# Kernel tuning notes

Hardware: AMD Instinct MI355X
Metric: run time of the kernel (lower is better)

Reference implementation:

```python
import jax, jax.numpy as jnp
import numpy as np

N = 100000  # number of nodes
SELF_LOOP_W = 2.0  # improved=True in PyG GCNConv


def gcn_conv(x, edge_index, W, b):
    # x: [N, Fin], edge_index: [2, E] (row=src, col=dst), W: [Fin, Fout], b: [Fout]
    src, dst = edge_index[0], edge_index[1]
    h = x @ W  # [N, Fout]
    # degree with improved self-loops (weight 2.0)
    ones = jnp.ones(src.shape, dtype=h.dtype)
    deg = jax.ops.segment_sum(ones, dst, num_segments=N) + SELF_LOOP_W
    dinv = jnp.where(deg > 0, jax.lax.rsqrt(deg), 0.0)
    norm = dinv[src] * dinv[dst]  # [E]
    agg = jax.ops.segment_sum(h[src] * norm[:, None], dst, num_segments=N)
    # self-loop contribution: weight 2.0, norm = dinv_i * 2 * dinv_i
    agg = agg + h * (SELF_LOOP_W * dinv * dinv)[:, None]
    return agg + b


def setup_inputs() -> dict:
    key = jax.random.key(0)
    ks = jax.random.split(key, 6)
    x = jax.random.normal(ks[0], (N, 64), dtype=jnp.float32)
    edge_index = jax.random.randint(ks[1], (2, 1600000), 0, N, dtype=jnp.int64)
    W1 = jax.random.normal(ks[2], (64, 64), dtype=jnp.float32) * 0.1
    b1 = jax.random.normal(ks[3], (64,), dtype=jnp.float32) * 0.1
    W2 = jax.random.normal(ks[4], (64, 32), dtype=jnp.float32) * 0.1
    b2 = jax.random.normal(ks[5], (32,), dtype=jnp.float32) * 0.1
    return {"x": x, "edge_index": edge_index, "W1": W1, "b1": b1, "W2": W2, "b2": b2}


def reference(x, edge_index, W1, b1, W2, b2):
    h1 = jax.nn.relu(gcn_conv(x, edge_index, W1, b1))
    feature_map = h1
    out = gcn_conv(h1, edge_index, W2, b2)
    return (out, feature_map)
```

## Files before the change

kernel.cpp:

```cpp
#include <hip/hip_runtime.h>

#define N_NODES 100000
#define E_EDGES 1600000

#define BSHIFT 7
#define BSIZE 128
#define NBUCK ((N_NODES + BSIZE - 1) / BSIZE)
#define STAGE_TPB 512
#define STAGE_EPT 8
#define STAGE_CHUNK (STAGE_TPB * STAGE_EPT)
#define NREP 2
#define BUCKET_CAP 4096
#define CSR_STRIDE (BUCKET_CAP + 512)

typedef __attribute__((ext_vector_type(8))) short short8;
typedef __attribute__((ext_vector_type(4))) float float4v;
typedef __attribute__((ext_vector_type(4))) int int4v;
typedef __attribute__((ext_vector_type(4))) unsigned uint4v;

__device__ inline unsigned short f2bf(float f) {
    union { float f; unsigned u; } t; t.f = f;
    unsigned r = (t.u + 0x7fffu + ((t.u >> 16) & 1u)) >> 16;
    return (unsigned short)r;
}
__device__ inline float bf2f(unsigned short h) {
    union { unsigned u; float f; } t; t.u = ((unsigned)h) << 16; return t.f;
}
__device__ inline unsigned pack_bf16x2(float a, float b) {
    return (unsigned)f2bf(a) | ((unsigned)f2bf(b) << 16);
}
__device__ inline float bf_lo(unsigned u) { union { unsigned u; float f; } t; t.u = u << 16; return t.f; }
__device__ inline float bf_hi(unsigned u) { union { unsigned u; float f; } t; t.u = u & 0xffff0000u; return t.f; }

__global__ void cursor_init_kernel(int* __restrict__ gcursor,
                                   unsigned* __restrict__ HS1, unsigned* __restrict__ HS2) {
    int b = blockIdx.x * blockDim.x + threadIdx.x;
    if (b < NBUCK) gcursor[b] = b * BUCKET_CAP;
    if (b < 32) HS1[(size_t)N_NODES * 32 + b] = 0u;
    if (b < 16) HS2[(size_t)N_NODES * 16 + b] = 0u;
}

__global__ void __launch_bounds__(STAGE_TPB) stage_kernel(
    const int* __restrict__ src, const int* __restrict__ dst,
    int* __restrict__ gcursor, unsigned* __restrict__ staged, int E) {
    __shared__ int hist[NREP][NBUCK];
    __shared__ int dbase[NBUCK];
    __shared__ int scanw[1024];
    __shared__ unsigned lrec[STAGE_CHUNK];
    __shared__ int laddr[STAGE_CHUNK];
    const int tid = threadIdx.x;
    const int rep = (tid >> 8) & (NREP - 1);
    const int e0 = blockIdx.x * STAGE_CHUNK;
    for (int i = tid; i < NREP * NBUCK; i += STAGE_TPB) ((int*)hist)[i] = 0;
    scanw[tid] = 0; scanw[tid + 512] = 0;
    __syncthreads();
    int d[STAGE_EPT], s[STAGE_EPT];
#pragma unroll
    for (int k = 0; k < STAGE_EPT / 4; ++k) {
        int e = e0 + (k * STAGE_TPB + tid) * 4;
        if (e < E) {
            int4v sv = __builtin_nontemporal_load((const int4v*)(src + e));
            int4v dv = __builtin_nontemporal_load((const int4v*)(dst + e));
#pragma unroll
            for (int i = 0; i < 4; ++i) {
                s[4 * k + i] = sv[i];
                d[4 * k + i] = dv[i];
                atomicAdd(&hist[rep][dv[i] >> BSHIFT], 1);
            }
        } else {
#pragma unroll
            for (int i = 0; i < 4; ++i) d[4 * k + i] = -1;
        }
    }
    __syncthreads();
    for (int i = tid; i < NBUCK; i += STAGE_TPB) scanw[i] = hist[0][i] + hist[1][i];
    if (tid + 512 < NBUCK) scanw[tid + 512] = hist[0][tid + 512] + hist[1][tid + 512];
    __syncthreads();
    for (int off = 1; off < 1024; off <<= 1) {
        int v0 = (tid >= off) ? scanw[tid - off] : 0;
        int v1 = (tid + 512 >= off) ? scanw[tid + 512 - off] : 0;
        __syncthreads();
        scanw[tid] += v0;
        scanw[tid + 512] += v1;
        __syncthreads();
    }
    for (int i = tid; i < NBUCK; i += STAGE_TPB) {
        int h0 = hist[0][i], h1 = hist[1][i];
        int t = h0 + h1;
        int excl = scanw[i] - t;
        if (t > 0) {
            int g = atomicAdd(&gcursor[i], t);
            dbase[i] = g - excl;
        }
        hist[0][i] = excl;
        hist[1][i] = excl + h0;
    }
    __syncthreads();
#pragma unroll
    for (int k = 0; k < STAGE_EPT; ++k) {
        if (d[k] >= 0) {
            int b = d[k] >> BSHIFT;
            int slot = atomicAdd(&hist[rep][b], 1);
            lrec[slot] = (unsigned)s[k] | ((unsigned)(d[k] & (BSIZE - 1)) << 17);
            laddr[slot] = dbase[b] + slot;
        }
    }
    __syncthreads();
    const int total = min(STAGE_CHUNK, E - e0);
    for (int i = tid; i < total; i += STAGE_TPB) {
        int a = laddr[i];
        if ((unsigned)a < (unsigned)(NBUCK * BUCKET_CAP))
            staged[a] = lrec[i];
    }
}

__global__ void bucket_csr_kernel(const unsigned* __restrict__ staged,
                                  const int* __restrict__ gcursor,
                                  int4v* __restrict__ meta, float* __restrict__ dinv,
                                  int* __restrict__ csrc, int n) {
    __shared__ int ldeg[BSIZE];
    __shared__ int laex[BSIZE];
    __shared__ int lscan[BSIZE];
    __shared__ int lcnt[BSIZE];
    __shared__ int h2[32];
    __shared__ int c2[32];
    __shared__ unsigned lrec[BUCKET_CAP];
    __shared__ int lsrc[BUCKET_CAP + 512];
    __shared__ int ltot;
    const int b = blockIdx.x;
    const int node0 = b * BSIZE;
    const int nn = min(BSIZE, n - node0);
    const int tid = threadIdx.x;
    if (tid < BSIZE) { ldeg[tid] = 0; lcnt[tid] = 0; }
    if (tid < 32) { h2[tid] = 0; c2[tid] = 0; }
    __syncthreads();
    const int ebase = b * CSR_STRIDE;
    int ecnt = gcursor[b] - b * BUCKET_CAP;
    if (ecnt > BUCKET_CAP) ecnt = BUCKET_CAP;
    const int sbase = b * BUCKET_CAP;
    for (int i = tid; i < ecnt; i += 256) {
        unsigned r = staged[sbase + i];
        lrec[i] = r;
        atomicAdd(&ldeg[(r >> 17) & (BSIZE - 1)], 1);
    }
    __syncthreads();
    int mydeg = (tid < BSIZE) ? ldeg[tid] : 0;
    int adeg = (mydeg + 3) & ~3;
    if (tid < BSIZE) lscan[tid] = adeg;
    __syncthreads();
    for (int off = 1; off < BSIZE; off <<= 1) {
        int v = 0;
        if (tid < BSIZE && tid >= off) v = lscan[tid - off];
        __syncthreads();
        if (tid < BSIZE) lscan[tid] += v;
        __syncthreads();
    }
    const int bin = min(adeg >> 2, 31);
    float mydinv = 0.0f;
    if (tid < BSIZE) {
        int aex = lscan[tid] - adeg;
        laex[tid] = aex;
        if (tid == BSIZE - 1) ltot = lscan[tid];
        if (tid < nn) {
            mydinv = rsqrtf((float)mydeg + 2.0f);
            dinv[node0 + tid] = mydinv;
            for (int k = mydeg; k < adeg; ++k) lsrc[aex + k] = N_NODES;
            atomicAdd(&h2[bin], 1);
        }
    }
    __syncthreads();
    if (tid == 0) {
        int acc = 0;
        for (int k = 0; k < 32; ++k) { int v = h2[k]; h2[k] = acc; acc += v; }
    }
    __syncthreads();
    if (tid < nn) {
        int pos = h2[bin] + atomicAdd(&c2[bin], 1);
        union { float f; int i; } dv; dv.f = mydinv;
        meta[node0 + pos] = (int4v){ebase + laex[tid], mydeg, node0 + tid, dv.i};
    }
    for (int i = tid; i < ecnt; i += 256) {
        unsigned r = lrec[i];
        int dl = (int)((r >> 17) & (BSIZE - 1));
        int sv = (int)(r & 0x1FFFFu);
        int pos = laex[dl] + atomicAdd(&lcnt[dl], 1);
        if (pos < BUCKET_CAP + 512) lsrc[pos] = sv;
    }
    __syncthreads();
    const int tot = ltot;
    for (int i = tid; i < tot; i += 256)
        csrc[ebase + i] = lsrc[i];
}

template <int FOUT>
__global__ void __launch_bounds__(256) linear_mfma_kernel(
    const float* __restrict__ X, const float* __restrict__ W,
    const float* __restrict__ dinv, unsigned* __restrict__ HS, int n) {
    constexpr int NT = FOUT / 16;
    constexpr int ROWU = NT * 8;
    const int NTILES_M = n / 16;
    const int lane = threadIdx.x & 63;
    const int gwave = blockIdx.x * 4 + (threadIdx.x >> 6);
    const int nwaves = gridDim.x * 4;
    const int m = lane & 15;
    const int q = lane >> 4;

    short8 Bhi[2][NT], Blo[2][NT];
#pragma unroll
    for (int ks = 0; ks < 2; ++ks)
#pragma unroll
        for (int nt = 0; nt < NT; ++nt) {
            short8 bh, bl;
#pragma unroll
            for (int j = 0; j < 8; ++j) {
                int k = ks * 32 + q * 8 + j;
                float wv = W[k * FOUT + nt * 16 + m];
                unsigned short h = f2bf(wv);
                bh[j] = (short)h;
                bl[j] = (short)f2bf(wv - bf2f(h));
            }
            Bhi[ks][nt] = bh;
            Blo[ks][nt] = bl;
        }

    for (int tile = gwave; tile < NTILES_M; tile += nwaves) {
        const int row0 = tile * 16;
        float4v C[NT];
#pragma unroll
        for (int nt = 0; nt < NT; ++nt) C[nt] = (float4v){0.f, 0.f, 0.f, 0.f};
#pragma unroll
        for (int ks = 0; ks < 2; ++ks) {
            const float* xp = X + (size_t)(row0 + m) * 64 + ks * 32 + q * 8;
            float4v x0 = __builtin_nontemporal_load((const float4v*)xp);
            float4v x1 = __builtin_nontemporal_load((const float4v*)(xp + 4));
            short8 Ahi, Alo;
#pragma unroll
            for (int j = 0; j < 4; ++j) {
                unsigned short h0 = f2bf(x0[j]);
                Ahi[j] = (short)h0;
                Alo[j] = (short)f2bf(x0[j] - bf2f(h0));
                unsigned short h1 = f2bf(x1[j]);
                Ahi[4 + j] = (short)h1;
                Alo[4 + j] = (short)f2bf(x1[j] - bf2f(h1));
            }
#pragma unroll
            for (int nt = 0; nt < NT; ++nt) {
                C[nt] = __builtin_amdgcn_mfma_f32_16x16x32_bf16(Ahi, Bhi[ks][nt], C[nt], 0, 0, 0);
                C[nt] = __builtin_amdgcn_mfma_f32_16x16x32_bf16(Alo, Bhi[ks][nt], C[nt], 0, 0, 0);
                C[nt] = __builtin_amdgcn_mfma_f32_16x16x32_bf16(Ahi, Blo[ks][nt], C[nt], 0, 0, 0);
            }
        }
#pragma unroll
        for (int ch = 0; ch < NT / 2; ++ch) {
#pragma unroll
            for (int reg = 0; reg < 4; ++reg) {
                int r = row0 + q * 4 + reg;
                float di = dinv[r];
                unsigned u = pack_bf16x2(C[2 * ch][reg] * di, C[2 * ch + 1][reg] * di);
                __builtin_nontemporal_store(u, HS + (size_t)r * ROWU + ch * 16 + m);
            }
        }
    }
}

template <int ROWU, bool RELU>
__global__ void __launch_bounds__(256) gather_vec_kernel(
    const int4v* __restrict__ meta, const int* __restrict__ csrc,
    const unsigned* __restrict__ HS, const float* __restrict__ bias,
    float* __restrict__ OUT, int n) {
    constexpr int G = ROWU / 4;
    constexpr int NPB = 256 / G;
    constexpr int FOUT = ROWU * 2;
    const int gslot = blockIdx.x * NPB + (int)(threadIdx.x / G);
    const int t = threadIdx.x % G;
    if (gslot >= n) return;
    const int4v mi = meta[gslot];
    const int start = mi[0];
    const int deg = mi[1];
    const int node = mi[2];
    union { int i; float f; } dv; dv.i = mi[3];
    const float dd = dv.f;
    const int pend = start + ((deg + 3) & ~3);
    const unsigned* __restrict__ HSt = HS + 4 * t;
    const uint4v own = *(const uint4v*)(HS + (size_t)node * ROWU + 4 * t);
    float alo[4], ahi[4];
#pragma unroll
    for (int k = 0; k < 4; ++k) { alo[k] = 2.0f * bf_lo(own[k]); ahi[k] = 2.0f * bf_hi(own[k]); }
    int j = start;
    for (; j + 8 <= pend; j += 8) {
        int4v s0 = __builtin_nontemporal_load((const int4v*)(csrc + j));
        int4v s1 = __builtin_nontemporal_load((const int4v*)(csrc + j + 4));
        uint4v u0 = *(const uint4v*)(HSt + (size_t)s0[0] * ROWU);
        uint4v u1 = *(const uint4v*)(HSt + (size_t)s0[1] * ROWU);
        uint4v u2 = *(const uint4v*)(HSt + (size_t)s0[2] * ROWU);
        uint4v u3 = *(const uint4v*)(HSt + (size_t)s0[3] * ROWU);
        uint4v u4 = *(const uint4v*)(HSt + (size_t)s1[0] * ROWU);
        uint4v u5 = *(const uint4v*)(HSt + (size_t)s1[1] * ROWU);
        uint4v u6 = *(const uint4v*)(HSt + (size_t)s1[2] * ROWU);
        uint4v u7 = *(const uint4v*)(HSt + (size_t)s1[3] * ROWU);
#pragma unroll
        for (int k = 0; k < 4; ++k) {
            float l01 = bf_lo(u0[k]) + bf_lo(u1[k]);
            float l23 = bf_lo(u2[k]) + bf_lo(u3[k]);
            float l45 = bf_lo(u4[k]) + bf_lo(u5[k]);
            float l67 = bf_lo(u6[k]) + bf_lo(u7[k]);
            alo[k] += (l01 + l23) + (l45 + l67);
            float h01 = bf_hi(u0[k]) + bf_hi(u1[k]);
            float h23 = bf_hi(u2[k]) + bf_hi(u3[k]);
            float h45 = bf_hi(u4[k]) + bf_hi(u5[k]);
            float h67 = bf_hi(u6[k]) + bf_hi(u7[k]);
            ahi[k] += (h01 + h23) + (h45 + h67);
        }
    }
    if (j < pend) {
        int4v s0 = __builtin_nontemporal_load((const int4v*)(csrc + j));
        uint4v u0 = *(const uint4v*)(HSt + (size_t)s0[0] * ROWU);
        uint4v u1 = *(const uint4v*)(HSt + (size_t)s0[1] * ROWU);
        uint4v u2 = *(const uint4v*)(HSt + (size_t)s0[2] * ROWU);
        uint4v u3 = *(const uint4v*)(HSt + (size_t)s0[3] * ROWU);
#pragma unroll
        for (int k = 0; k < 4; ++k) {
            alo[k] += (bf_lo(u0[k]) + bf_lo(u1[k])) + (bf_lo(u2[k]) + bf_lo(u3[k]));
            ahi[k] += (bf_hi(u0[k]) + bf_hi(u1[k])) + (bf_hi(u2[k]) + bf_hi(u3[k]));
        }
    }
    const int ch = t >> 2;
    const int c0 = (4 * t) & 15;
    const float4v blv = *(const float4v*)(bias + 32 * ch + c0);
    const float4v bhv = *(const float4v*)(bias + 32 * ch + 16 + c0);
    float4v olo, ohi;
#pragma unroll
    for (int k = 0; k < 4; ++k) {
        float o0 = alo[k] * dd + blv[k];
        float o1 = ahi[k] * dd + bhv[k];
        if (RELU) { o0 = fmaxf(o0, 0.0f); o1 = fmaxf(o1, 0.0f); }
        olo[k] = o0;
        ohi[k] = o1;
    }
    float* op = OUT + (size_t)node * FOUT + 32 * ch + c0;
    __builtin_nontemporal_store(olo, (float4v*)op);
    __builtin_nontemporal_store(ohi, (float4v*)(op + 16));
}

extern "C" void kernel_launch(void* const* d_in, const int* in_sizes, int n_in,
                              void* d_out, int out_size, void* d_ws, size_t ws_size,
                              hipStream_t stream) {
    const float* x  = (const float*)d_in[0];
    const int*   ei = (const int*)d_in[1];
    const float* W1 = (const float*)d_in[2];
    const float* b1 = (const float*)d_in[3];
    const float* W2 = (const float*)d_in[4];
    const float* b2 = (const float*)d_in[5];

    const int* srcp = ei;
    const int* dstp = ei + E_EDGES;

    float* out = (float*)d_out;
    float* fm  = (float*)d_out + N_NODES * 32;

    char* w = (char*)d_ws;
    auto alloc = [&w](size_t bytes) -> void* {
        uintptr_t p = ((uintptr_t)w + 255) & ~(uintptr_t)255;
        w = (char*)(p + bytes);
        return (void*)p;
    };
    int*      gcursor  = (int*)alloc(sizeof(int) * NBUCK);
    int4v*    meta     = (int4v*)alloc(sizeof(int4v) * N_NODES);
    float*    dinv     = (float*)alloc(sizeof(float) * N_NODES);
    int*      csrc     = (int*)alloc(sizeof(int) * (size_t)NBUCK * CSR_STRIDE);
    unsigned* staged   = (unsigned*)alloc(sizeof(unsigned) * (size_t)NBUCK * BUCKET_CAP);
    unsigned* HS1      = (unsigned*)alloc(sizeof(unsigned) * (size_t)(N_NODES + 1) * 32);
    unsigned* HS2      = (unsigned*)alloc(sizeof(unsigned) * (size_t)(N_NODES + 1) * 16);

    cursor_init_kernel<<<(NBUCK + 255) / 256, 256, 0, stream>>>(gcursor, HS1, HS2);
    stage_kernel<<<(E_EDGES + STAGE_CHUNK - 1) / STAGE_CHUNK, STAGE_TPB, 0, stream>>>(
        srcp, dstp, gcursor, staged, E_EDGES);
    bucket_csr_kernel<<<NBUCK, 256, 0, stream>>>(staged, gcursor, meta, dinv, csrc, N_NODES);

    linear_mfma_kernel<64><<<512, 256, 0, stream>>>(x, W1, dinv, HS1, N_NODES);
    gather_vec_kernel<32, true><<<(N_NODES + 31) / 32, 256, 0, stream>>>(
        meta, csrc, HS1, b1, fm, N_NODES);

    linear_mfma_kernel<32><<<512, 256, 0, stream>>>(fm, W2, dinv, HS2, N_NODES);
    gather_vec_kernel<16, false><<<(N_NODES + 63) / 64, 256, 0, stream>>>(
        meta, csrc, HS2, b2, out, N_NODES);
}
```

Baseline: 199.2 us.

## Reuse first-pass atomic ranks for scatter slots and drop cursor init kernel

The return value of the histogram atomicAdd is now kept as a per-edge rank in both the staging and bucket-CSR kernels. Scatter positions are then computed from the prefix offsets plus that rank, which removes the second round of shared-memory atomics. The cursor init kernel is replaced by a hipMemsetAsync, with bucket bases folded into dbase, and the sentinel row zeroing moves into the linear kernel. Nontemporal load and store hints are added for the staged and CSR buffers. The cost is an extra per-edge rank array in registers and LDS.

```diff
diff --git a/kernel.cpp b/kernel.cpp
--- a/kernel.cpp
+++ b/kernel.cpp
@@ -32,18 +32,11 @@
 __device__ inline float bf_lo(unsigned u) { union { unsigned u; float f; } t; t.u = u << 16; return t.f; }
 __device__ inline float bf_hi(unsigned u) { union { unsigned u; float f; } t; t.u = u & 0xffff0000u; return t.f; }
 
-__global__ void cursor_init_kernel(int* __restrict__ gcursor,
-                                   unsigned* __restrict__ HS1, unsigned* __restrict__ HS2) {
-    int b = blockIdx.x * blockDim.x + threadIdx.x;
-    if (b < NBUCK) gcursor[b] = b * BUCKET_CAP;
-    if (b < 32) HS1[(size_t)N_NODES * 32 + b] = 0u;
-    if (b < 16) HS2[(size_t)N_NODES * 16 + b] = 0u;
-}
-
 __global__ void __launch_bounds__(STAGE_TPB) stage_kernel(
     const int* __restrict__ src, const int* __restrict__ dst,
     int* __restrict__ gcursor, unsigned* __restrict__ staged, int E) {
     __shared__ int hist[NREP][NBUCK];
+    __shared__ int excl[NBUCK];
     __shared__ int dbase[NBUCK];
     __shared__ int scanw[1024];
     __shared__ unsigned lrec[STAGE_CHUNK];
@@ -52,9 +45,8 @@
     const int rep = (tid >> 8) & (NREP - 1);
     const int e0 = blockIdx.x * STAGE_CHUNK;
     for (int i = tid; i < NREP * NBUCK; i += STAGE_TPB) ((int*)hist)[i] = 0;
-    scanw[tid] = 0; scanw[tid + 512] = 0;
-    __syncthreads();
-    int d[STAGE_EPT], s[STAGE_EPT];
+    __syncthreads();
+    int d[STAGE_EPT], s[STAGE_EPT], rk[STAGE_EPT];
 #pragma unroll
     for (int k = 0; k < STAGE_EPT / 4; ++k) {
         int e = e0 + (k * STAGE_TPB + tid) * 4;
@@ -65,7 +57,7 @@
             for (int i = 0; i < 4; ++i) {
                 s[4 * k + i] = sv[i];
                 d[4 * k + i] = dv[i];
-                atomicAdd(&hist[rep][dv[i] >> BSHIFT], 1);
+                rk[4 * k + i] = atomicAdd(&hist[rep][dv[i] >> BSHIFT], 1);
             }
         } else {
 #pragma unroll
@@ -73,8 +65,8 @@
         }
     }
     __syncthreads();
-    for (int i = tid; i < NBUCK; i += STAGE_TPB) scanw[i] = hist[0][i] + hist[1][i];
-    if (tid + 512 < NBUCK) scanw[tid + 512] = hist[0][tid + 512] + hist[1][tid + 512];
+    scanw[tid] = (tid < NBUCK) ? hist[0][tid] + hist[1][tid] : 0;
+    scanw[tid + 512] = (tid + 512 < NBUCK) ? hist[0][tid + 512] + hist[1][tid + 512] : 0;
     __syncthreads();
     for (int off = 1; off < 1024; off <<= 1) {
         int v0 = (tid >= off) ? scanw[tid - off] : 0;
@@ -85,22 +77,20 @@
         __syncthreads();
     }
     for (int i = tid; i < NBUCK; i += STAGE_TPB) {
-        int h0 = hist[0][i], h1 = hist[1][i];
-        int t = h0 + h1;
-        int excl = scanw[i] - t;
+        int t = hist[0][i] + hist[1][i];
+        int ex = scanw[i] - t;
+        excl[i] = ex;
         if (t > 0) {
             int g = atomicAdd(&gcursor[i], t);
-            dbase[i] = g - excl;
-        }
-        hist[0][i] = excl;
-        hist[1][i] = excl + h0;
+            dbase[i] = i * BUCKET_CAP + g - ex;
+        }
     }
     __syncthreads();
 #pragma unroll
     for (int k = 0; k < STAGE_EPT; ++k) {
         if (d[k] >= 0) {
             int b = d[k] >> BSHIFT;
-            int slot = atomicAdd(&hist[rep][b], 1);
+            int slot = excl[b] + (rep ? hist[0][b] : 0) + rk[k];
             lrec[slot] = (unsigned)s[k] | ((unsigned)(d[k] & (BSIZE - 1)) << 17);
             laddr[slot] = dbase[b] + slot;
         }
@@ -121,27 +111,27 @@
     __shared__ int ldeg[BSIZE];
     __shared__ int laex[BSIZE];
     __shared__ int lscan[BSIZE];
-    __shared__ int lcnt[BSIZE];
     __shared__ int h2[32];
     __shared__ int c2[32];
     __shared__ unsigned lrec[BUCKET_CAP];
+    __shared__ unsigned short lrnk[BUCKET_CAP];
     __shared__ int lsrc[BUCKET_CAP + 512];
     __shared__ int ltot;
     const int b = blockIdx.x;
     const int node0 = b * BSIZE;
     const int nn = min(BSIZE, n - node0);
     const int tid = threadIdx.x;
-    if (tid < BSIZE) { ldeg[tid] = 0; lcnt[tid] = 0; }
+    if (tid < BSIZE) ldeg[tid] = 0;
     if (tid < 32) { h2[tid] = 0; c2[tid] = 0; }
     __syncthreads();
     const int ebase = b * CSR_STRIDE;
-    int ecnt = gcursor[b] - b * BUCKET_CAP;
+    int ecnt = gcursor[b];
     if (ecnt > BUCKET_CAP) ecnt = BUCKET_CAP;
     const int sbase = b * BUCKET_CAP;
     for (int i = tid; i < ecnt; i += 256) {
-        unsigned r = staged[sbase + i];
+        unsigned r = __builtin_nontemporal_load(staged + sbase + i);
         lrec[i] = r;
-        atomicAdd(&ldeg[(r >> 17) & (BSIZE - 1)], 1);
+        lrnk[i] = (unsigned short)atomicAdd(&ldeg[(r >> 17) & (BSIZE - 1)], 1);
     }
     __syncthreads();
     int mydeg = (tid < BSIZE) ? ldeg[tid] : 0;
@@ -182,14 +172,13 @@
     for (int i = tid; i < ecnt; i += 256) {
         unsigned r = lrec[i];
         int dl = (int)((r >> 17) & (BSIZE - 1));
-        int sv = (int)(r & 0x1FFFFu);
-        int pos = laex[dl] + atomicAdd(&lcnt[dl], 1);
-        if (pos < BUCKET_CAP + 512) lsrc[pos] = sv;
+        int pos = laex[dl] + (int)lrnk[i];
+        if (pos < BUCKET_CAP + 512) lsrc[pos] = (int)(r & 0x1FFFFu);
     }
     __syncthreads();
     const int tot = ltot;
     for (int i = tid; i < tot; i += 256)
-        csrc[ebase + i] = lsrc[i];
+        __builtin_nontemporal_store(lsrc[i], csrc + ebase + i);
 }
 
 template <int FOUT>
@@ -204,6 +193,8 @@
     const int nwaves = gridDim.x * 4;
     const int m = lane & 15;
     const int q = lane >> 4;
+    if (blockIdx.x == 0 && threadIdx.x < ROWU)
+        HS[(size_t)n * ROWU + threadIdx.x] = 0u;
 
     short8 Bhi[2][NT], Blo[2][NT];
 #pragma unroll
@@ -372,7 +363,7 @@
     unsigned* HS1      = (unsigned*)alloc(sizeof(unsigned) * (size_t)(N_NODES + 1) * 32);
     unsigned* HS2      = (unsigned*)alloc(sizeof(unsigned) * (size_t)(N_NODES + 1) * 16);
 
-    cursor_init_kernel<<<(NBUCK + 255) / 256, 256, 0, stream>>>(gcursor, HS1, HS2);
+    hipMemsetAsync(gcursor, 0, sizeof(int) * NBUCK, stream);
     stage_kernel<<<(E_EDGES + STAGE_CHUNK - 1) / STAGE_CHUNK, STAGE_TPB, 0, stream>>>(
         srcp, dstp, gcursor, staged, E_EDGES);
     bucket_csr_kernel<<<NBUCK, 256, 0, stream>>>(staged, gcursor, meta, dinv, csrc, N_NODES);
```

After: 205.1 us. +2.9%, slower.
